# Kernel tuning notes

Hardware: AMD Instinct MI355X
Metric: run time of the kernel (lower is better)

## Reference

```python
import jax, jax.numpy as jnp
import numpy as np

B, S, D, H, E, K = 4, 1024, 1024, 16, 8, 2
DH = D // H
FF = 4 * D  # expert hidden dim
EPS = 1e-5


def _layernorm(x, g, b):
    mu = jnp.mean(x, axis=-1, keepdims=True)
    var = jnp.mean(jnp.square(x - mu), axis=-1, keepdims=True)
    return (x - mu) / jnp.sqrt(var + EPS) * g + b


def setup_inputs() -> dict:
    key = jax.random.key(0)
    ks = jax.random.split(key, 16)
    s = 0.02
    return {
        "x": jax.random.normal(ks[0], (B, S, D), jnp.float32),
        "mask": jnp.ones((B, S), jnp.int32),
        "ln1_g": jnp.ones((D,), jnp.float32),
        "ln1_b": jnp.zeros((D,), jnp.float32),
        "ln2_g": jnp.ones((D,), jnp.float32),
        "ln2_b": jnp.zeros((D,), jnp.float32),
        "wq": jax.random.normal(ks[1], (D, D), jnp.float32) * s,
        "bq": jnp.zeros((D,), jnp.float32),
        "wk": jax.random.normal(ks[2], (D, D), jnp.float32) * s,
        "bk": jnp.zeros((D,), jnp.float32),
        "wv": jax.random.normal(ks[3], (D, D), jnp.float32) * s,
        "bv": jnp.zeros((D,), jnp.float32),
        "wo": jax.random.normal(ks[4], (D, D), jnp.float32) * s,
        "bo": jnp.zeros((D,), jnp.float32),
        "w_router": jax.random.normal(ks[5], (D, E), jnp.float32) * s,
        "b_router": jnp.zeros((E,), jnp.float32),
        "w1": jax.random.normal(ks[6], (E, D, FF), jnp.float32) * s,
        "b1": jnp.zeros((E, FF), jnp.float32),
        "w2": jax.random.normal(ks[7], (E, FF, D), jnp.float32) * s,
        "b2": jnp.zeros((E, D), jnp.float32),
    }


def _forward(x, mask, ln1_g, ln1_b, ln2_g, ln2_b, wq, bq, wk, bk, wv, bv,
             wo, bo, w_router, b_router, w1, b1, w2, b2):
    scale = DH ** -0.5
    # --- attention sub-block (pre-LN) ---
    xn = _layernorm(x, ln1_g, ln1_b)
    q = (xn @ wq + bq).reshape(B, S, H, DH).transpose(0, 2, 1, 3)  # [B,H,S,DH]
    k = (xn @ wk + bk).reshape(B, S, H, DH).transpose(0, 2, 1, 3)
    v = (xn @ wv + bv).reshape(B, S, H, DH).transpose(0, 2, 1, 3)
    scores = jnp.einsum('bhqd,bhkd->bhqk', q, k) * scale
    scores = jnp.where(mask[:, None, None, :] == 0, -jnp.inf, scores)
    attn = jax.nn.softmax(scores, axis=-1)
    ao = jnp.einsum('bhqk,bhkd->bhqd', attn, v)
    ao = ao.transpose(0, 2, 1, 3).reshape(B, S, D) @ wo + bo
    x = x + ao  # dropout is identity in eval
    # --- MoE sub-block ---
    xn2 = _layernorm(x, ln2_g, ln2_b)
    logits = xn2 @ w_router + b_router          # [B,S,E]
    top_v, top_i = jax.lax.top_k(logits, K)     # [B,S,K]
    probs = jax.nn.softmax(top_v, axis=-1)      # softmax over top-k logits
    # dense combine weight per expert: sum_k prob_k * onehot(idx_k)
    combine = jnp.sum(jax.nn.one_hot(top_i, E, dtype=xn2.dtype) * probs[..., None], axis=-2)  # [B,S,E]
    h = jax.nn.gelu(jnp.einsum('bsd,edh->ebsh', xn2, w1) + b1[:, None, None, :], approximate=False)
    eo = jnp.einsum('ebsh,ehd->ebsd', h, w2) + b2[:, None, None, :]   # [E,B,S,D]
    moe_out = jnp.einsum('bse,ebsd->bsd', combine, eo)
    return x + moe_out


def reference(x, mask, ln1_g, ln1_b, ln2_g, ln2_b, wq, bq, wk, bk, wv, bv,
              wo, bo, w_router, b_router, w1, b1, w2, b2):
    return _forward(x, mask, ln1_g, ln1_b, ln2_g, ln2_b, wq, bq, wk, bk, wv,
                    bv, wo, bo, w_router, b_router, w1, b1, w2, b2)
```

## Files before the change

kernel.cpp:

```cpp
#include <hip/hip_runtime.h>
#include <hip/hip_bf16.h>
#include <cmath>

typedef __hip_bfloat16 bf16;
typedef float f32x4 __attribute__((ext_vector_type(4)));
typedef int   i32x4 __attribute__((ext_vector_type(4)));

#define DEV static __device__ __forceinline__

constexpr int BB   = 4;
constexpr int SS   = 1024;
constexpr int DM   = 1024;
constexpr int HH   = 16;
constexpr int DHD  = 64;
constexpr int NEXP = 8;
constexpr int FFD  = 4096;
constexpr int NTOK = BB*SS;
constexpr int CAP  = NTOK*2 + NEXP*128;

DEV float bf2f(unsigned short u){ union{unsigned int i; float f;} z; z.i=((unsigned int)u)<<16; return z.f; }
DEV unsigned short f2bf(float f){ bf16 h = __float2bfloat16(f); return __builtin_bit_cast(unsigned short, h); }

DEV void stage16(const void* g, void* lds_base_uniform) {
  __builtin_amdgcn_global_load_lds(
      (const __attribute__((address_space(1))) void*)g,
      (__attribute__((address_space(3))) void*)lds_base_uniform,
      16, 0, 0);
}

template<int BM,int BN,int EPI,bool EXPERT,bool GATHER,bool OUT_SLOT,int NPASS=1,int ZMODE=0>
__global__ __launch_bounds__((BM/64)*(BN/64)*64)
void et_gemm(const bf16* __restrict__ A, const bf16* __restrict__ Bt, void* __restrict__ Cout,
             const float* __restrict__ bias, const float* __restrict__ res,
             int Kdim, int lda, int ldb, int ldc,
             long abs_, long bbs_, long cbs_, float scale,
             const int* __restrict__ pad_off, const int* __restrict__ slots,
             long psA, long psB, float* __restrict__ Cf, int bias_zs)
{
  constexpr int WN = BN/64, WM = BM/64, NW = WM*WN;
  constexpr int CA = (BM/16)/NW, CB = (BN/16)/NW;
  const int tid = threadIdx.x, wid = tid>>6, lane = tid&63;

  const int gx = gridDim.x, gy = gridDim.y;
  const long nwg = (long)gx*gy*gridDim.z;
  long lin = blockIdx.x + (long)gx*(blockIdx.y + (long)gy*blockIdx.z);
  {
    const long q = nwg >> 3, r = nwg & 7;
    const long xcd = lin & 7, idx = lin >> 3;
    lin = (xcd < r ? xcd*(q+1) : r*(q+1) + (xcd-r)*q) + idx;
  }
  const int bxi = (int)(lin % gx);
  const long rem = lin / gx;
  const int byi = (int)(rem % gy);
  const int bzi = (int)(rem / gy);

  const int row0 = bxi*BM, col0 = byi*BN;
  const int z = bzi;
  int off0 = 0;
  if constexpr (EXPERT) {
    off0 = pad_off[z];
    const int rows = pad_off[z+1] - off0;
    if (row0 >= rows) return;
  }
  long coff;
  if constexpr (ZMODE==1) {
    const long hb = (long)(z>>4)*SS*DM + (long)(z&15)*64;
    A += hb; Bt += hb; coff = (long)z*SS*SS;
  } else if constexpr (ZMODE==2) {
    A  += (long)z*SS*SS;
    Bt += (long)z*DHD*SS;
    coff = (long)(z>>4)*SS*DM + (long)(z&15)*64;
  } else {
    if constexpr (!EXPERT) A += (size_t)z * abs_;
    Bt += (size_t)z * bbs_;
    coff = (long)z*cbs_;
  }
  const long bofs = (long)z * bias_zs;

  const int sr = lane>>2;
  const int sk = (lane&3)*8;

  long arow[CA];
  #pragma unroll
  for (int i=0;i<CA;i++){
    const int r = (wid + i*NW)*16 + sr;
    if constexpr (GATHER)      arow[i] = slots[off0 + row0 + r];
    else if constexpr (EXPERT) arow[i] = off0 + row0 + r;
    else                       arow[i] = row0 + r;
  }
  int brow[CB];
  #pragma unroll
  for (int i=0;i<CB;i++) brow[i] = col0 + (wid + i*NW)*16 + sr;

  const int wm = wid / WN, wn = wid % WN;
  const int fr = lane & 15, fg = lane >> 4;

  f32x4 acc[4][4];
  #pragma unroll
  for (int m=0;m<4;m++)
    #pragma unroll
    for (int n=0;n<4;n++) acc[m][n] = (f32x4)(0.f);

  if constexpr (NPASS==3) {
    __shared__ __align__(16) bf16 As[2][2][BM*32];
    __shared__ __align__(16) bf16 Bs[2][2][BN*32];
    auto STG = [&](int buf, int kt) {
      #pragma unroll
      for (int i=0;i<CA;i++){
        stage16(A +        arow[i]*(long)lda + kt + sk, (void*)&As[buf][0][(wid + i*NW)*512]);
        stage16(A + psA +  arow[i]*(long)lda + kt + sk, (void*)&As[buf][1][(wid + i*NW)*512]);
      }
      #pragma unroll
      for (int i=0;i<CB;i++){
        stage16(Bt +       (long)brow[i]*ldb + kt + sk, (void*)&Bs[buf][0][(wid + i*NW)*512]);
        stage16(Bt + psB + (long)brow[i]*ldb + kt + sk, (void*)&Bs[buf][1][(wid + i*NW)*512]);
      }
    };
    const int nsteps = Kdim >> 5;
    int cur = 0;
    STG(0, 0);
    __syncthreads();
    for (int s = 0; s < nsteps; s++) {
      if (s + 1 < nsteps) STG(cur^1, (s+1)*32);
      i32x4 a0[4], a1[4], b0[4], b1[4];
      #pragma unroll
      for (int m=0;m<4;m++) {
        a0[m] = *(const i32x4*)&As[cur][0][(wm*64 + m*16 + fr)*32 + fg*8];
        a1[m] = *(const i32x4*)&As[cur][1][(wm*64 + m*16 + fr)*32 + fg*8];
      }
      #pragma unroll
      for (int n=0;n<4;n++) {
        b0[n] = *(const i32x4*)&Bs[cur][0][(wn*64 + n*16 + fr)*32 + fg*8];
        b1[n] = *(const i32x4*)&Bs[cur][1][(wn*64 + n*16 + fr)*32 + fg*8];
      }
      asm volatile("s_nop 1" ::);
      #pragma unroll
      for (int m=0;m<4;m++)
        #pragma unroll
        for (int n=0;n<4;n++) {
          asm("v_mfma_f32_16x16x32_bf16 %0, %1, %2, %0"
              : "+v"(acc[m][n]) : "v"(a0[m]), "v"(b0[n]));
          asm("v_mfma_f32_16x16x32_bf16 %0, %1, %2, %0"
              : "+v"(acc[m][n]) : "v"(a0[m]), "v"(b1[n]));
          asm("v_mfma_f32_16x16x32_bf16 %0, %1, %2, %0"
              : "+v"(acc[m][n]) : "v"(a1[m]), "v"(b0[n]));
        }
      __syncthreads();
      cur ^= 1;
    }
  } else {
    __shared__ __align__(16) bf16 As[2][BM*32];
    __shared__ __align__(16) bf16 Bs[2][BN*32];
    auto STAGE = [&](int buf, int kt) {
      #pragma unroll
      for (int i=0;i<CA;i++)
        stage16(A + arow[i]*(long)lda + kt + sk, (void*)&As[buf][(wid + i*NW)*512]);
      #pragma unroll
      for (int i=0;i<CB;i++)
        stage16(Bt + (long)brow[i]*ldb + kt + sk, (void*)&Bs[buf][(wid + i*NW)*512]);
    };
    const int nsteps = Kdim >> 5;
    int cur = 0;
    STAGE(0, 0);
    __syncthreads();
    for (int s = 0; s < nsteps; s++) {
      if (s + 1 < nsteps) STAGE(cur^1, (s+1)*32);
      i32x4 av[4], bv[4];
      #pragma unroll
      for (int m=0;m<4;m++) av[m] = *(const i32x4*)&As[cur][(wm*64 + m*16 + fr)*32 + fg*8];
      #pragma unroll
      for (int n=0;n<4;n++) bv[n] = *(const i32x4*)&Bs[cur][(wn*64 + n*16 + fr)*32 + fg*8];
      asm volatile("s_nop 1" ::);
      #pragma unroll
      for (int m=0;m<4;m++)
        #pragma unroll
        for (int n=0;n<4;n++)
          asm("v_mfma_f32_16x16x32_bf16 %0, %1, %2, %0"
              : "+v"(acc[m][n]) : "v"(av[m]), "v"(bv[n]));
      __syncthreads();
      cur ^= 1;
    }
  }

  #pragma unroll
  for (int m=0;m<4;m++)
    #pragma unroll
    for (int n=0;n<4;n++)
      asm volatile("s_nop 7\n\ts_nop 7" : "+v"(acc[m][n]) ::);

  const long rbase = (EXPERT && OUT_SLOT) ? (long)(off0 + row0) : (long)row0;
  #pragma unroll
  for (int m=0;m<4;m++) {
    #pragma unroll
    for (int n=0;n<4;n++) {
      #pragma unroll
      for (int j=0;j<4;j++) {
        const long r = rbase + wm*64 + m*16 + fg*4 + j;
        const long c = col0 + wn*64 + n*16 + fr;
        const size_t ci = (size_t)coff + (size_t)r*ldc + c;
        float v = acc[m][n][j];
        if constexpr (EPI==0) {
          ((bf16*)Cout)[ci] = __float2bfloat16(v + bias[bofs + c]);
        } else if constexpr (EPI==1) {
          ((bf16*)Cout)[ci] = __float2bfloat16(v*scale);
        } else if constexpr (EPI==2) {
          ((float*)Cout)[ci] = v + bias[bofs + c] + res[(size_t)r*ldc + c];
        } else if constexpr (EPI==3) {
          const float t = v + bias[bofs + c];
          ((bf16*)Cout)[ci] = __float2bfloat16(0.5f*t*(1.0f+erff(t*0.70710678118654752f)));
        } else {
          const float t = v + bias[bofs + c];
          ((bf16*)Cout)[ci] = __float2bfloat16(t);
          Cf[ci] = t;
        }
      }
    }
  }
}

template<typename T>
__global__ __launch_bounds__(256)
void et_transpose(const T* __restrict__ in, bf16* __restrict__ outp,
                  int ldin, int ldout, long in_bs, long out_bs)
{
  __shared__ float tile[64][65];
  const int z = blockIdx.z;
  in   += (size_t)z * in_bs;
  outp += (size_t)z * out_bs;
  const int r0 = blockIdx.x*64, c0 = blockIdx.y*64;
  const int tid = threadIdx.x;
  #pragma unroll
  for (int i=0;i<4;i++) {
    const int idx = tid*4 + i*1024;
    const int r = idx>>6, c = idx&63;
    if constexpr (sizeof(T)==4) {
      const float4 v = *(const float4*)&in[(size_t)(r0+r)*ldin + c0 + c];
      tile[r][c]=v.x; tile[r][c+1]=v.y; tile[r][c+2]=v.z; tile[r][c+3]=v.w;
    } else {
      const ushort4 v = *(const ushort4*)&in[(size_t)(r0+r)*ldin + c0 + c];
      tile[r][c]=bf2f(v.x); tile[r][c+1]=bf2f(v.y); tile[r][c+2]=bf2f(v.z); tile[r][c+3]=bf2f(v.w);
    }
  }
  __syncthreads();
  #pragma unroll
  for (int i=0;i<4;i++) {
    const int idx = tid*4 + i*1024;
    const int c = idx>>6, r = idx&63;
    ushort4 o;
    o.x=f2bf(tile[r][c]); o.y=f2bf(tile[r+1][c]); o.z=f2bf(tile[r+2][c]); o.w=f2bf(tile[r+3][c]);
    *(ushort4*)&outp[(size_t)(c0+c)*ldout + r0 + r] = o;
  }
}

template<typename TI, typename TO>
__global__ __launch_bounds__(256)
void k_trans_head(const TI* __restrict__ in, TO* __restrict__ outp)
{
  __shared__ float tile[64][65];
  const int z = blockIdx.z;
  in   += (size_t)(z>>4)*SS*DM + (size_t)(z&15)*64;
  outp += (size_t)z*DHD*SS;
  const int r0 = blockIdx.x*64;
  const int tid = threadIdx.x;
  #pragma unroll
  for (int i=0;i<4;i++) {
    const int idx = tid*4 + i*1024;
    const int r = idx>>6, c = idx&63;
    if constexpr (sizeof(TI)==4) {
      const float4 v = *(const float4*)&in[(size_t)(r0+r)*DM + c];
      tile[r][c]=v.x; tile[r][c+1]=v.y; tile[r][c+2]=v.z; tile[r][c+3]=v.w;
    } else {
      const ushort4 v = *(const ushort4*)&in[(size_t)(r0+r)*DM + c];
      tile[r][c]=bf2f(v.x); tile[r][c+1]=bf2f(v.y); tile[r][c+2]=bf2f(v.z); tile[r][c+3]=bf2f(v.w);
    }
  }
  __syncthreads();
  #pragma unroll
  for (int i=0;i<4;i++) {
    const int idx = tid*4 + i*1024;
    const int c = idx>>6, r = idx&63;
    if constexpr (sizeof(TO)==4) {
      float4 o;
      o.x=tile[r][c]; o.y=tile[r+1][c]; o.z=tile[r+2][c]; o.w=tile[r+3][c];
      *(float4*)&outp[(size_t)c*SS + r0 + r] = o;
    } else {
      ushort4 o;
      o.x=f2bf(tile[r][c]); o.y=f2bf(tile[r+1][c]); o.z=f2bf(tile[r+2][c]); o.w=f2bf(tile[r+3][c]);
      *(ushort4*)&outp[(size_t)c*SS + r0 + r] = o;
    }
  }
}

__global__ __launch_bounds__(256)
void et_transpose2(const float* __restrict__ in0, const float* __restrict__ in1,
                   const float* __restrict__ in2, bf16* __restrict__ outp,
                   int ldin, int ldout, long pstride, long out_zs)
{
  __shared__ float tile[64][65];
  const int z = blockIdx.z;
  const float* in = (z==0) ? in0 : (z==1) ? in1 : in2;
  outp += (size_t)z * out_zs;
  const int r0 = blockIdx.x*64, c0 = blockIdx.y*64;
  const int tid = threadIdx.x;
  #pragma unroll
  for (int i=0;i<4;i++) {
    const int idx = tid*4 + i*1024;
    const int r = idx>>6, c = idx&63;
    const float4 v = *(const float4*)&in[(size_t)(r0+r)*ldin + c0 + c];
    tile[r][c]=v.x; tile[r][c+1]=v.y; tile[r][c+2]=v.z; tile[r][c+3]=v.w;
  }
  __syncthreads();
  #pragma unroll
  for (int i=0;i<4;i++) {
    const int idx = tid*4 + i*1024;
    const int c = idx>>6, r = idx&63;
    ushort4 o0, o1;
    unsigned short* p0 = (unsigned short*)&o0;
    unsigned short* p1 = (unsigned short*)&o1;
    #pragma unroll
    for (int j=0;j<4;j++) {
      float v = tile[r+j][c];
      const unsigned short h0 = f2bf(v);
      p0[j] = h0;
      v -= bf2f(h0);
      p1[j] = f2bf(v);
    }
    const size_t oi = (size_t)(c0+c)*ldout + r0 + r;
    *(ushort4*)&outp[oi] = o0;
    *(ushort4*)&outp[oi + pstride] = o1;
  }
}

__global__ __launch_bounds__(256)
void et_ln2(const float* __restrict__ xin, const float* __restrict__ g,
            const float* __restrict__ bsh, bf16* __restrict__ outp, long pstride)
{
  const int row = blockIdx.x, tid = threadIdx.x;
  const float4 v = ((const float4*)(xin + (size_t)row*DM))[tid];
  float s = v.x+v.y+v.z+v.w;
  #pragma unroll
  for (int o=32;o;o>>=1) s += __shfl_xor(s,o);
  __shared__ float s4[4], q4[4];
  if ((tid&63)==0) s4[tid>>6]=s;
  __syncthreads();
  const float mu = (s4[0]+s4[1]+s4[2]+s4[3]) * (1.f/DM);
  const float d0=v.x-mu,d1=v.y-mu,d2=v.z-mu,d3=v.w-mu;
  float q = d0*d0+d1*d1+d2*d2+d3*d3;
  #pragma unroll
  for (int o=32;o;o>>=1) q += __shfl_xor(q,o);
  if ((tid&63)==0) q4[tid>>6]=q;
  __syncthreads();
  const float var = (q4[0]+q4[1]+q4[2]+q4[3]) * (1.f/DM);
  const float rstd = rsqrtf(var + 1e-5f);
  const float4 gg = ((const float4*)g)[tid];
  const float4 bb = ((const float4*)bsh)[tid];
  float of[4];
  of[0] = d0*rstd*gg.x + bb.x;
  of[1] = d1*rstd*gg.y + bb.y;
  of[2] = d2*rstd*gg.z + bb.z;
  of[3] = d3*rstd*gg.w + bb.w;
  ushort4 p0, p1;
  unsigned short* pp0 = (unsigned short*)&p0;
  unsigned short* pp1 = (unsigned short*)&p1;
  #pragma unroll
  for (int k=0;k<4;k++) {
    float vv = of[k];
    const unsigned short h0 = f2bf(vv); pp0[k] = h0;
    vv -= bf2f(h0);
    pp1[k] = f2bf(vv);
  }
  const size_t oi = (size_t)row*DM;
  ((ushort4*)(outp + oi))[tid] = p0;
  ((ushort4*)(outp + pstride + oi))[tid] = p1;
}

__global__ __launch_bounds__(256)
void et_softmax(bf16* __restrict__ scp, const int* __restrict__ mask)
{
  const int row = blockIdx.x, tid = threadIdx.x;
  const int b = row >> 14;
  bf16* rp = scp + (size_t)row*SS;
  const int* mrow = mask + (size_t)b*SS;
  const ushort4 u = ((const ushort4*)rp)[tid];
  const int4 mv = ((const int4*)mrow)[tid];
  float f0 = bf2f(u.x), f1 = bf2f(u.y), f2 = bf2f(u.z), f3 = bf2f(u.w);
  if (mv.x==0) f0 = -1e30f;
  if (mv.y==0) f1 = -1e30f;
  if (mv.z==0) f2 = -1e30f;
  if (mv.w==0) f3 = -1e30f;
  float m = fmaxf(fmaxf(f0,f1),fmaxf(f2,f3));
  #pragma unroll
  for (int o=32;o;o>>=1) m = fmaxf(m, __shfl_xor(m,o));
  __shared__ float sm[4], ssum[4];
  if ((tid&63)==0) sm[tid>>6] = m;
  __syncthreads();
  m = fmaxf(fmaxf(sm[0],sm[1]),fmaxf(sm[2],sm[3]));
  const float e0 = __expf(f0-m), e1 = __expf(f1-m), e2 = __expf(f2-m), e3 = __expf(f3-m);
  float s = e0+e1+e2+e3;
  #pragma unroll
  for (int o=32;o;o>>=1) s += __shfl_xor(s,o);
  if ((tid&63)==0) ssum[tid>>6] = s;
  __syncthreads();
  s = ssum[0]+ssum[1]+ssum[2]+ssum[3];
  const float ri = 1.0f/s;
  ushort4 o4;
  o4.x = f2bf(e0*ri); o4.y = f2bf(e1*ri); o4.z = f2bf(e2*ri); o4.w = f2bf(e3*ri);
  ((ushort4*)rp)[tid] = o4;
}

__global__ __launch_bounds__(256)
void et_router2(const float* __restrict__ x1, const float* __restrict__ g,
                const float* __restrict__ bsh, const float* __restrict__ wr,
                const float* __restrict__ br, bf16* __restrict__ xn2,
                int* __restrict__ t2e, float* __restrict__ t2p,
                int* __restrict__ flaglist, int* __restrict__ cntb)
{
  const int wid = threadIdx.x>>6, lane = threadIdx.x&63;
  const int t = blockIdx.x*4 + wid;
  const float* xr = x1 + (size_t)t*DM;
  float4 xv[4];
  float s = 0.f;
  #pragma unroll
  for (int p=0;p<4;p++){
    xv[p] = *(const float4*)&xr[p*256 + lane*4];
    s += xv[p].x+xv[p].y+xv[p].z+xv[p].w;
  }
  #pragma unroll
  for (int o=32;o;o>>=1) s += __shfl_xor(s,o);
  const float mu = s * (1.f/DM);
  float q = 0.f;
  #pragma unroll
  for (int p=0;p<4;p++){
    const float a=xv[p].x-mu,b=xv[p].y-mu,c=xv[p].z-mu,d=xv[p].w-mu;
    q += a*a+b*b+c*c+d*d;
  }
  #pragma unroll
  for (int o=32;o;o>>=1) q += __shfl_xor(q,o);
  const float rstd = rsqrtf(q*(1.f/DM) + 1e-5f);
  float acc[NEXP];
  #pragma unroll
  for (int e=0;e<NEXP;e++) acc[e]=0.f;
  #pragma unroll
  for (int p=0;p<4;p++){
    const int d0 = p*256 + lane*4;
    const float4 gg = *(const float4*)&g[d0];
    const float4 bb = *(const float4*)&bsh[d0];
    float xn[4];
    xn[0]=(xv[p].x-mu)*rstd*gg.x+bb.x;
    xn[1]=(xv[p].y-mu)*rstd*gg.y+bb.y;
    xn[2]=(xv[p].z-mu)*rstd*gg.z+bb.z;
    xn[3]=(xv[p].w-mu)*rstd*gg.w+bb.w;
    ushort4 xo;
    xo.x=f2bf(xn[0]); xo.y=f2bf(xn[1]); xo.z=f2bf(xn[2]); xo.w=f2bf(xn[3]);
    *(ushort4*)&xn2[(size_t)t*DM + d0] = xo;
    #pragma unroll
    for (int j=0;j<4;j++){
      const float4 w0  = ((const float4*)&wr[(size_t)(d0+j)*NEXP])[0];
      const float4 w1v = ((const float4*)&wr[(size_t)(d0+j)*NEXP])[1];
      acc[0]+=xn[j]*w0.x;  acc[1]+=xn[j]*w0.y;  acc[2]+=xn[j]*w0.z;  acc[3]+=xn[j]*w0.w;
      acc[4]+=xn[j]*w1v.x; acc[5]+=xn[j]*w1v.y; acc[6]+=xn[j]*w1v.z; acc[7]+=xn[j]*w1v.w;
    }
  }
  #pragma unroll
  for (int e=0;e<NEXP;e++)
    #pragma unroll
    for (int o=32;o;o>>=1) acc[e] += __shfl_xor(acc[e],o);
  if (lane==0) {
    float v0=-1e30f, v1=-1e30f, v2=-1e30f; int e0=0, e1=0;
    #pragma unroll
    for (int e=0;e<NEXP;e++) {
      const float v = acc[e] + br[e];
      if (v>v0){v2=v1;v1=v0;e1=e0;v0=v;e0=e;}
      else if (v>v1){v2=v1;v1=v;e1=e;}
      else if (v>v2){v2=v;}
    }
    const float dd = __expf(v1-v0);
    const float p0 = 1.f/(1.f+dd);
    t2e[t*2]=e0; t2e[t*2+1]=e1;
    t2p[t*2]=p0; t2p[t*2+1]=dd*p0;
    if (v1 - v2 < 0.02f) {
      const int b = t >> 10;
      const int ib = atomicAdd(&cntb[b], 1);
      flaglist[b*1024 + ib] = t;
    }
  }
}

__global__ __launch_bounds__(256)
void k_rec4(const float* __restrict__ qf, const float* __restrict__ kfT,
            const float* __restrict__ vf, const int* __restrict__ flaglist,
            const int* __restrict__ cntb, const int* __restrict__ mask,
            float* __restrict__ aoF)
{
  const int h = blockIdx.y, b = blockIdx.z;
  const int tid = threadIdx.x, lane = tid&63, wv_ = tid>>6;
  const int nb = cntb[b];
  __shared__ float qs[4][64];
  __shared__ float scb[4][SS];
  __shared__ float part[4][4][64];
  __shared__ float tsum[4];
  const int* mrow = mask + (size_t)b*SS;
  const float* kbase = kfT + ((size_t)(b*HH + h)*DHD)*SS + tid;
  const float* vbase = vf + (size_t)b*SS*DM + h*64 + lane;

  for (int t0 = blockIdx.x*4; t0 < nb; t0 += gridDim.x*4) {
    const int nt = min(4, nb - t0);
    for (int idx = tid; idx < 4*64; idx += 256) {
      const int j = idx >> 6, d = idx & 63;
      float qv = 0.f;
      if (j < nt) {
        const int t = flaglist[b*1024 + t0 + j];
        qv = qf[(size_t)t*DM + h*64 + d];
      }
      qs[j][d] = qv;
    }
    __syncthreads();
    float a00=0,a01=0,a02=0,a03=0, a10=0,a11=0,a12=0,a13=0;
    float a20=0,a21=0,a22=0,a23=0, a30=0,a31=0,a32=0,a33=0;
    #pragma unroll 4
    for (int u=0; u<64; u++) {
      const float* kr = kbase + (size_t)u*SS;
      const float k0 = kr[0], k1 = kr[256], k2 = kr[512], k3 = kr[768];
      const float q0 = qs[0][u], q1 = qs[1][u], q2 = qs[2][u], q3 = qs[3][u];
      a00 += q0*k0; a01 += q0*k1; a02 += q0*k2; a03 += q0*k3;
      a10 += q1*k0; a11 += q1*k1; a12 += q1*k2; a13 += q1*k3;
      a20 += q2*k0; a21 += q2*k1; a22 += q2*k2; a23 += q2*k3;
      a30 += q3*k0; a31 += q3*k1; a32 += q3*k2; a33 += q3*k3;
    }
    const bool m0 = mrow[tid]!=0, m1 = mrow[tid+256]!=0, m2 = mrow[tid+512]!=0, m3 = mrow[tid+768]!=0;
    scb[0][tid]=m0?a00*0.125f:-1e30f; scb[0][tid+256]=m1?a01*0.125f:-1e30f;
    scb[0][tid+512]=m2?a02*0.125f:-1e30f; scb[0][tid+768]=m3?a03*0.125f:-1e30f;
    scb[1][tid]=m0?a10*0.125f:-1e30f; scb[1][tid+256]=m1?a11*0.125f:-1e30f;
    scb[1][tid+512]=m2?a12*0.125f:-1e30f; scb[1][tid+768]=m3?a13*0.125f:-1e30f;
    scb[2][tid]=m0?a20*0.125f:-1e30f; scb[2][tid+256]=m1?a21*0.125f:-1e30f;
    scb[2][tid+512]=m2?a22*0.125f:-1e30f; scb[2][tid+768]=m3?a23*0.125f:-1e30f;
    scb[3][tid]=m0?a30*0.125f:-1e30f; scb[3][tid+256]=m1?a31*0.125f:-1e30f;
    scb[3][tid+512]=m2?a32*0.125f:-1e30f; scb[3][tid+768]=m3?a33*0.125f:-1e30f;
    __syncthreads();
    {
      const int j = wv_;
      float v[16];
      float lm = -1e30f;
      #pragma unroll
      for (int kk=0;kk<16;kk++) { v[kk] = scb[j][lane + kk*64]; lm = fmaxf(lm, v[kk]); }
      #pragma unroll
      for (int o=32;o;o>>=1) lm = fmaxf(lm, __shfl_xor(lm,o));
      float ls = 0.f;
      #pragma unroll
      for (int kk=0;kk<16;kk++) {
        const float e = expf(v[kk]-lm);
        scb[j][lane + kk*64] = e; ls += e;
      }
      #pragma unroll
      for (int o=32;o;o>>=1) ls += __shfl_xor(ls,o);
      if (lane==0) tsum[j] = ls;
    }
    __syncthreads();
    float p0=0.f, p1=0.f, p2=0.f, p3=0.f;
    for (int s = wv_*4; s < SS; s += 16) {
      const float v0 = vbase[(size_t) s   *DM];
      const float v1 = vbase[(size_t)(s+1)*DM];
      const float v2 = vbase[(size_t)(s+2)*DM];
      const float v3 = vbase[(size_t)(s+3)*DM];
      p0 += scb[0][s]*v0 + scb[0][s+1]*v1 + scb[0][s+2]*v2 + scb[0][s+3]*v3;
      p1 += scb[1][s]*v0 + scb[1][s+1]*v1 + scb[1][s+2]*v2 + scb[1][s+3]*v3;
      p2 += scb[2][s]*v0 + scb[2][s+1]*v1 + scb[2][s+2]*v2 + scb[2][s+3]*v3;
      p3 += scb[3][s]*v0 + scb[3][s+1]*v1 + scb[3][s+2]*v2 + scb[3][s+3]*v3;
    }
    part[wv_][0][lane] = p0;
    part[wv_][1][lane] = p1;
    part[wv_][2][lane] = p2;
    part[wv_][3][lane] = p3;
    __syncthreads();
    for (int idx = tid; idx < nt*64; idx += 256) {
      const int j = idx >> 6, d = idx & 63;
      aoF[(size_t)(b*1024 + t0 + j)*DM + h*64 + d] =
        (part[0][j][d]+part[1][j][d]+part[2][j][d]+part[3][j][d]) / tsum[j];
    }
    __syncthreads();
  }
}

__global__ __launch_bounds__(256)
void k_flag_proj2(const float* __restrict__ aoF, const float* __restrict__ wo,
                  const float* __restrict__ bo, const float* __restrict__ x,
                  const int* __restrict__ flaglist, const int* __restrict__ cntb,
                  float* __restrict__ yF)
{
  const int tile = blockIdx.x;
  const int b = tile >> 7;
  const int i0 = (tile & 127) * 8;
  const int nb = cntb[b];
  if (i0 >= nb) return;
  const int nt = min(8, nb - i0);
  const int c0 = blockIdx.y * 128;
  const int tid = threadIdx.x;
  const int c = c0 + (tid & 127);
  const int dh = tid >> 7;
  __shared__ float ar[8][DM];
  __shared__ float ph[2][8][128];
  for (int k = tid; k < 8*256; k += 256) {
    const int j = k >> 8, q4i = k & 255;
    float4 v = make_float4(0.f,0.f,0.f,0.f);
    if (j < nt) v = ((const float4*)(aoF + (size_t)(b*1024 + i0 + j)*DM))[q4i];
    ((float4*)ar[j])[q4i] = v;
  }
  __syncthreads();
  float acc0=0.f, acc1=0.f, acc2=0.f, acc3=0.f;
  float acc4=0.f, acc5=0.f, acc6=0.f, acc7=0.f;
  const int dbase = dh*512;
  #pragma unroll 4
  for (int d=0; d<512; d++) {
    const float w = wo[(size_t)(dbase+d)*DM + c];
    acc0 += ar[0][dbase+d]*w; acc1 += ar[1][dbase+d]*w;
    acc2 += ar[2][dbase+d]*w; acc3 += ar[3][dbase+d]*w;
    acc4 += ar[4][dbase+d]*w; acc5 += ar[5][dbase+d]*w;
    acc6 += ar[6][dbase+d]*w; acc7 += ar[7][dbase+d]*w;
  }
  const int lc = tid & 127;
  ph[dh][0][lc]=acc0; ph[dh][1][lc]=acc1; ph[dh][2][lc]=acc2; ph[dh][3][lc]=acc3;
  ph[dh][4][lc]=acc4; ph[dh][5][lc]=acc5; ph[dh][6][lc]=acc6; ph[dh][7][lc]=acc7;
  __syncthreads();
  for (int k = tid; k < nt*128; k += 256) {
    const int j = k >> 7, ccl = k & 127;
    const int cc = c0 + ccl;
    const int slot = b*1024 + i0 + j;
    const int t = flaglist[slot];
    yF[(size_t)slot*DM + cc] = ph[0][j][ccl] + ph[1][j][ccl] + bo[cc] + x[(size_t)t*DM + cc];
  }
}

__global__ __launch_bounds__(256)
void k_flag_router(const float* __restrict__ yF, const float* __restrict__ g,
                   const float* __restrict__ bsh, const float* __restrict__ wr,
                   const float* __restrict__ br, const int* __restrict__ flaglist,
                   const int* __restrict__ cntb, int* __restrict__ t2e,
                   float* __restrict__ t2p)
{
  const int tid = threadIdx.x, lane = tid&63, wv_ = tid>>6;
  __shared__ float s4[4], q4[4], pt[4][8];
  for (int idx = blockIdx.x; idx < NTOK; idx += gridDim.x) {
    const int b = idx >> 10, ib = idx & 1023;
    if (ib >= cntb[b]) continue;
    const int t = flaglist[idx];
    const float4 v = ((const float4*)(yF + (size_t)idx*DM))[tid];
    float s = v.x+v.y+v.z+v.w;
    #pragma unroll
    for (int o=32;o;o>>=1) s += __shfl_xor(s,o);
    if (lane==0) s4[wv_]=s;
    __syncthreads();
    const float mu = (s4[0]+s4[1]+s4[2]+s4[3])*(1.f/DM);
    const float d0=v.x-mu, d1=v.y-mu, d2=v.z-mu, d3=v.w-mu;
    float q = d0*d0+d1*d1+d2*d2+d3*d3;
    #pragma unroll
    for (int o=32;o;o>>=1) q += __shfl_xor(q,o);
    if (lane==0) q4[wv_]=q;
    __syncthreads();
    const float var = (q4[0]+q4[1]+q4[2]+q4[3])*(1.f/DM);
    const float rstd = 1.0f/sqrtf(var + 1e-5f);
    const int dbase = tid*4;
    const float4 gg = ((const float4*)g)[tid];
    const float4 bb = ((const float4*)bsh)[tid];
    const float x0 = d0*rstd*gg.x+bb.x, x1_ = d1*rstd*gg.y+bb.y;
    const float x2 = d2*rstd*gg.z+bb.z, x3_ = d3*rstd*gg.w+bb.w;
    float pl[8];
    #pragma unroll
    for (int e=0;e<8;e++)
      pl[e] = x0*wr[(size_t)(dbase+0)*8+e] + x1_*wr[(size_t)(dbase+1)*8+e]
            + x2*wr[(size_t)(dbase+2)*8+e] + x3_*wr[(size_t)(dbase+3)*8+e];
    #pragma unroll
    for (int e=0;e<8;e++)
      #pragma unroll
      for (int o=32;o;o>>=1) pl[e] += __shfl_xor(pl[e],o);
    if (lane==0) {
      #pragma unroll
      for (int e=0;e<8;e++) pt[wv_][e]=pl[e];
    }
    __syncthreads();
    if (tid==0) {
      float v0=-1e30f, v1=-1e30f; int e0=0, e1=0;
      for (int e=0;e<8;e++) {
        const float L = pt[0][e]+pt[1][e]+pt[2][e]+pt[3][e] + br[e];
        if (L>v0){v1=v0;e1=e0;v0=L;e0=e;}
        else if (L>v1){v1=L;e1=e;}
      }
      const float dd=expf(v1-v0), p0=1.f/(1.f+dd);
      t2e[t*2]=e0; t2e[t*2+1]=e1;
      t2p[t*2]=p0; t2p[t*2+1]=dd*p0;
    }
    __syncthreads();
  }
}

__global__ void et_init(const float* __restrict__ bq, const float* __restrict__ bk,
                        const float* __restrict__ bv, float* __restrict__ bcat,
                        int* __restrict__ cnt)
{
  const int i = blockIdx.x*256 + threadIdx.x;
  if (i < 16) cnt[i]=0;
  if (i < DM) { bcat[i]=bq[i]; bcat[DM+i]=bk[i]; bcat[2*DM+i]=bv[i]; }
}

__global__ void et_count(const int* __restrict__ t2e, int* __restrict__ cnt)
{
  const int t = blockIdx.x*256 + threadIdx.x;
  if (t < NTOK) {
    atomicAdd(&cnt[t2e[t*2]], 1);
    atomicAdd(&cnt[t2e[t*2+1]], 1);
  }
}

__global__ void et_scan(const int* __restrict__ cnt, int* __restrict__ poff,
                        int* __restrict__ fil, int* __restrict__ slots)
{
  const int tid = threadIdx.x;
  if (tid==0) {
    int o=0;
    for (int e=0;e<NEXP;e++){ poff[e]=o; o += ((cnt[e]+127)>>7)<<7; }
    poff[NEXP]=o;
  }
  if (tid<NEXP) fil[tid]=0;
  for (int i=tid;i<CAP;i+=256) slots[i]=0;
}

__global__ void et_fill(const int* __restrict__ t2e, const int* __restrict__ poff,
                        int* __restrict__ fil, int* __restrict__ slots, int* __restrict__ sof)
{
  const int t = blockIdx.x*256 + threadIdx.x;
  if (t >= NTOK) return;
  #pragma unroll
  for (int kk=0;kk<2;kk++) {
    const int e = t2e[t*2+kk];
    const int pos = atomicAdd(&fil[e], 1);
    const int sl = poff[e] + pos;
    slots[sl] = t;
    sof[t*2+kk] = sl;
  }
}

__global__ __launch_bounds__(256)
void et_combine(const float* __restrict__ x1, const bf16* __restrict__ eo,
                const float* __restrict__ t2p, const int* __restrict__ sof,
                float* __restrict__ outp)
{
  const int t = blockIdx.x, tid = threadIdx.x;
  const int s0 = sof[t*2], s1 = sof[t*2+1];
  const float p0 = t2p[t*2], p1 = t2p[t*2+1];
  const float4 xv = ((const float4*)(x1 + (size_t)t*DM))[tid];
  const ushort4 a = ((const ushort4*)(eo + (size_t)s0*DM))[tid];
  const ushort4 c = ((const ushort4*)(eo + (size_t)s1*DM))[tid];
  float4 o;
  o.x = xv.x + p0*bf2f(a.x) + p1*bf2f(c.x);
  o.y = xv.y + p0*bf2f(a.y) + p1*bf2f(c.y);
  o.z = xv.z + p0*bf2f(a.z) + p1*bf2f(c.z);
  o.w = xv.w + p0*bf2f(a.w) + p1*bf2f(c.w);
  ((float4*)(outp + (size_t)t*DM))[tid] = o;
}

extern "C" void kernel_launch(void* const* d_in, const int* in_sizes, int n_in,
                              void* d_out, int out_size, void* d_ws, size_t ws_size,
                              hipStream_t stream)
{
  (void)in_sizes; (void)n_in; (void)out_size; (void)ws_size;
  const float* x    = (const float*)d_in[0];
  const int*   mask = (const int*)  d_in[1];
  const float* ln1g = (const float*)d_in[2];
  const float* ln1b = (const float*)d_in[3];
  const float* ln2g = (const float*)d_in[4];
  const float* ln2b = (const float*)d_in[5];
  const float* wq   = (const float*)d_in[6];
  const float* bq   = (const float*)d_in[7];
  const float* wk   = (const float*)d_in[8];
  const float* bk   = (const float*)d_in[9];
  const float* wv   = (const float*)d_in[10];
  const float* bv   = (const float*)d_in[11];
  const float* wo   = (const float*)d_in[12];
  const float* bo   = (const float*)d_in[13];
  const float* wr   = (const float*)d_in[14];
  const float* br   = (const float*)d_in[15];
  const float* w1   = (const float*)d_in[16];
  const float* b1   = (const float*)d_in[17];
  const float* w2   = (const float*)d_in[18];
  const float* b2   = (const float*)d_in[19];
  float* outp = (float*)d_out;

  char* wsb = (char*)d_ws;
  size_t off = 0;
  auto alloc = [&](size_t bytes)->void* {
    void* p = wsb + off;
    off += (bytes + 255) & ~(size_t)255;
    return p;
  };
  const long WPS  = (long)DM*DM;
  const long XPS  = (long)NTOK*DM;
  const long EWS  = (long)DM*FFD;
  bf16*  wqT2  = (bf16*) alloc((size_t)2*WPS*2);
  bf16*  wkT2  = (bf16*) alloc((size_t)2*WPS*2);
  bf16*  wvT2  = (bf16*) alloc((size_t)2*WPS*2);
  bf16*  woT   = (bf16*) alloc((size_t)WPS*2);
  bf16*  w1Ta  = (bf16*) alloc((size_t)NEXP*EWS*2);
  bf16*  w2Ta  = (bf16*) alloc((size_t)NEXP*EWS*2);
  bf16*  xn2p  = (bf16*) alloc((size_t)2*XPS*2);
  bf16*  qb    = (bf16*) alloc((size_t)XPS*2);
  bf16*  kb    = (bf16*) alloc((size_t)XPS*2);
  bf16*  vb    = (bf16*) alloc((size_t)XPS*2);
  bf16*  vt    = (bf16*) alloc((size_t)XPS*2);
  float* qf    = (float*)alloc((size_t)XPS*4);
  float* kf    = (float*)alloc((size_t)XPS*4);
  float* vf    = (float*)alloc((size_t)XPS*4);
  float* kfT   = (float*)alloc((size_t)XPS*4);
  bf16*  aob   = (bf16*) alloc((size_t)XPS*2);
  float* x1    = (float*)alloc((size_t)XPS*4);
  bf16*  xn2   = (bf16*) alloc((size_t)XPS*2);
  bf16*  hbuf  = (bf16*) alloc((size_t)CAP*FFD*2);
  bf16*  eo    = (bf16*) alloc((size_t)CAP*DM*2);
  float* bcat  = (float*)alloc((size_t)3*DM*4);
  int*   t2e   = (int*)  alloc((size_t)NTOK*2*4);
  float* t2p   = (float*)alloc((size_t)NTOK*2*4);
  int*   slots = (int*)  alloc((size_t)CAP*4);
  int*   sof   = (int*)  alloc((size_t)NTOK*2*4);
  int*   flagl = (int*)  alloc((size_t)NTOK*4);
  int*   cnt   = (int*)  alloc(64);
  int*   fil   = (int*)  alloc(64);
  int*   poff  = (int*)  alloc(64);
  int*   cntb  = cnt + 8;
  bf16*  sc    = (bf16*) w1Ta;
  float* aoF   = (float*)qb;
  float* yF    = (float*)vb;

  const dim3 T256(256);

  et_init<<<4,T256,0,stream>>>(bq, bk, bv, bcat, cnt);
  et_transpose2<<<dim3(DM/64,DM/64,3),T256,0,stream>>>(wq, wk, wv, wqT2, DM, DM, WPS, 2*WPS);
  et_transpose<float><<<dim3(DM/64,DM/64,1),T256,0,stream>>>(wo, woT, DM, DM, 0, 0);

  et_ln2<<<NTOK,T256,0,stream>>>(x, ln1g, ln1b, xn2p, XPS);

  et_gemm<128,64,4,false,false,false,3,0><<<dim3(NTOK/128, DM/64, 3),dim3(128),0,stream>>>(
      xn2p, wqT2, qb, bcat, nullptr, DM, DM, DM, DM,
      0, 2*WPS, XPS, 1.f, nullptr, nullptr, XPS, WPS, qf, DM);

  k_trans_head<bf16,bf16><<<dim3(SS/64,1,BB*HH),T256,0,stream>>>(vb, vt);
  k_trans_head<float,float><<<dim3(SS/64,1,BB*HH),T256,0,stream>>>(kf, kfT);

  et_gemm<128,128,1,false,false,false,1,1><<<dim3(SS/128, SS/128, BB*HH),T256,0,stream>>>(
      qb, kb, sc, nullptr, nullptr, DHD, DM, DM, SS,
      0,0,0, 0.125f, nullptr,nullptr, 0,0,nullptr, 0);
  et_softmax<<<BB*HH*SS,T256,0,stream>>>(sc, mask);
  et_gemm<64,64,1,false,false,false,1,2><<<dim3(SS/64, 1, BB*HH),dim3(64),0,stream>>>(
      sc, vt, aob, nullptr, nullptr, SS, SS, SS, DM,
      0,0,0, 1.0f, nullptr,nullptr, 0,0,nullptr, 0);

  et_gemm<64,64,2,false,false,false,1,0><<<dim3(NTOK/64, DM/64, 1),dim3(64),0,stream>>>(
      aob, woT, x1, bo, x, DM, DM, DM, DM, 0,0,0, 1.f, nullptr,nullptr, 0,0,nullptr, 0);

  et_router2<<<NTOK/4,T256,0,stream>>>(x1, ln2g, ln2b, wr, br, xn2, t2e, t2p, flagl, cntb);
  k_rec4<<<dim3(32,HH,BB),T256,0,stream>>>(qf, kfT, vf, flagl, cntb, mask, aoF);
  k_flag_proj2<<<dim3(NTOK/8, DM/128),T256,0,stream>>>(aoF, wo, bo, x, flagl, cntb, yF);
  k_flag_router<<<1024,T256,0,stream>>>(yF, ln2g, ln2b, wr, br, flagl, cntb, t2e, t2p);

  et_count<<<NTOK/256,T256,0,stream>>>(t2e, cnt);
  et_scan<<<1,T256,0,stream>>>(cnt, poff, fil, slots);
  et_fill<<<NTOK/256,T256,0,stream>>>(t2e, poff, fil, slots, sof);

  et_transpose<float><<<dim3(DM/64, FFD/64, NEXP),T256,0,stream>>>(w1, w1Ta, FFD, DM, EWS, EWS);
  et_transpose<float><<<dim3(FFD/64, DM/64, NEXP),T256,0,stream>>>(w2, w2Ta, DM, FFD, EWS, EWS);

  et_gemm<128,128,3,true,true,true,1,0><<<dim3(NTOK/128, FFD/128, NEXP),T256,0,stream>>>(
      xn2, w1Ta, hbuf, b1, nullptr, DM, DM, DM, FFD,
      0, EWS, 0, 1.f, poff, slots, 0,0,nullptr, FFD);
  et_gemm<128,128,0,true,false,true,1,0><<<dim3(NTOK/128, DM/128, NEXP),T256,0,stream>>>(
      hbuf, w2Ta, eo, b2, nullptr, FFD, FFD, FFD, DM,
      0, EWS, 0, 1.f, poff, nullptr, 0,0,nullptr, DM);

  et_combine<<<NTOK,T256,0,stream>>>(x1, eo, t2p, sof, outp);
}
```

Baseline: 922.3 us.

## Fuse QK^T, softmax and PV into a single flash-attention kernel

Replaces the three-kernel attention path (score GEMM writing a full bf16 score matrix, row softmax kernel, PV GEMM) with one online-softmax kernel. Each block keeps a 64-row query tile in registers and streams K and V tiles through swizzled LDS. It computes scores with MFMA, tracks running max and sum per row, and accumulates the output. This removes the B*H*S*S score round trip to global memory and two kernel launches. In exchange, P is rounded to bf16 per tile, K/V loads are synchronous with no double buffering, and only 4 waves per block hide latency.

```diff
diff --git a/kernel.cpp b/kernel.cpp
--- a/kernel.cpp
+++ b/kernel.cpp
@@ -63,10 +63,7 @@
     if (row0 >= rows) return;
   }
   long coff;
-  if constexpr (ZMODE==1) {
-    const long hb = (long)(z>>4)*SS*DM + (long)(z&15)*64;
-    A += hb; Bt += hb; coff = (long)z*SS*SS;
-  } else if constexpr (ZMODE==2) {
+  if constexpr (ZMODE==2) {
     A  += (long)z*SS*SS;
     Bt += (long)z*DHD*SS;
     coff = (long)(z>>4)*SS*DM + (long)(z&15)*64;
@@ -218,6 +215,130 @@
   }
 }
 
+__global__ __launch_bounds__(256)
+void k_flash(const bf16* __restrict__ qb, const bf16* __restrict__ kb,
+             const bf16* __restrict__ vt, const int* __restrict__ mask,
+             bf16* __restrict__ aob)
+{
+  const int qt = blockIdx.x, h = blockIdx.y, b = blockIdx.z;
+  const int tid = threadIdx.x, wid = tid>>6, lane = tid&63;
+  const int fr = lane & 15, fg = lane >> 4;
+  __shared__ __align__(16) bf16 Ks[64*64];
+  __shared__ __align__(16) bf16 Vs[64*64];
+  __shared__ __align__(16) bf16 Pl[4][16*64];
+  const int q0 = qt*64;
+  const int qrow = q0 + wid*16 + fr;
+  i32x4 qreg[2];
+  #pragma unroll
+  for (int c=0;c<2;c++)
+    qreg[c] = *(const i32x4*)&qb[((size_t)(b*SS)+qrow)*DM + h*64 + c*32 + fg*8];
+  f32x4 oacc[4];
+  #pragma unroll
+  for (int n=0;n<4;n++) oacc[n]=(f32x4)(0.f);
+  float mrow[4], lrow[4];
+  #pragma unroll
+  for (int j=0;j<4;j++){ mrow[j]=-1e30f; lrow[j]=0.f; }
+
+  const int srow = lane>>3;
+  const int scolsw = ((lane&7) ^ srow)*8;
+  auto swz = [](int row, int coleb)->int {
+    return row*128 + (coleb ^ ((row&7)<<4));
+  };
+
+  for (int kt=0; kt<SS/64; kt++) {
+    const int kv0 = kt*64;
+    #pragma unroll
+    for (int i=0;i<2;i++) {
+      const int r = (wid*2+i)*8 + srow;
+      stage16(kb + ((size_t)(b*SS)+kv0+r)*DM + h*64 + scolsw, (void*)&Ks[(wid*2+i)*512]);
+      stage16(vt + ((size_t)(b*HH+h)*64 + r)*SS + kv0 + scolsw, (void*)&Vs[(wid*2+i)*512]);
+    }
+    __syncthreads();
+    f32x4 sacc[4];
+    #pragma unroll
+    for (int n=0;n<4;n++) sacc[n]=(f32x4)(0.f);
+    asm volatile("s_nop 1" ::);
+    #pragma unroll
+    for (int c=0;c<2;c++) {
+      i32x4 bk[4];
+      #pragma unroll
+      for (int n=0;n<4;n++)
+        bk[n] = *(const i32x4*)((const char*)Ks + swz(n*16+fr, c*64+fg*16));
+      #pragma unroll
+      for (int n=0;n<4;n++)
+        asm("v_mfma_f32_16x16x32_bf16 %0, %1, %2, %0"
+            : "+v"(sacc[n]) : "v"(qreg[c]), "v"(bk[n]));
+    }
+    #pragma unroll
+    for (int n=0;n<4;n++)
+      asm volatile("s_nop 7\n\ts_nop 7" : "+v"(sacc[n]) ::);
+    float sc[4][4];
+    #pragma unroll
+    for (int n=0;n<4;n++) {
+      const bool mm = mask[b*SS + kv0 + n*16 + fr] != 0;
+      #pragma unroll
+      for (int j=0;j<4;j++)
+        sc[n][j] = mm ? sacc[n][j]*0.125f : -1e30f;
+    }
+    float scale[4];
+    #pragma unroll
+    for (int j=0;j<4;j++) {
+      float tm = fmaxf(fmaxf(sc[0][j],sc[1][j]),fmaxf(sc[2][j],sc[3][j]));
+      #pragma unroll
+      for (int o=8;o;o>>=1) tm = fmaxf(tm, __shfl_xor(tm,o));
+      const float nm = fmaxf(mrow[j], tm);
+      scale[j] = __expf(mrow[j]-nm);
+      mrow[j] = nm;
+      float ts = 0.f;
+      #pragma unroll
+      for (int n=0;n<4;n++) { sc[n][j] = __expf(sc[n][j]-nm); ts += sc[n][j]; }
+      #pragma unroll
+      for (int o=8;o;o>>=1) ts += __shfl_xor(ts,o);
+      lrow[j] = lrow[j]*scale[j] + ts;
+    }
+    #pragma unroll
+    for (int n=0;n<4;n++)
+      asm volatile("s_nop 7\n\ts_nop 7" : "+v"(oacc[n]) ::);
+    #pragma unroll
+    for (int n=0;n<4;n++)
+      #pragma unroll
+      for (int j=0;j<4;j++) oacc[n][j] *= scale[j];
+    char* plw = (char*)Pl[wid];
+    #pragma unroll
+    for (int n=0;n<4;n++)
+      #pragma unroll
+      for (int j=0;j<4;j++) {
+        const int row = fg*4+j, col = n*16+fr;
+        *(bf16*)(plw + row*128 + ((col*2) ^ ((row&7)<<4))) = __float2bfloat16(sc[n][j]);
+      }
+    asm volatile("s_nop 1" ::);
+    #pragma unroll
+    for (int c=0;c<2;c++) {
+      i32x4 pa = *(const i32x4*)(plw + swz(fr, c*64+fg*16));
+      i32x4 bv[4];
+      #pragma unroll
+      for (int n=0;n<4;n++)
+        bv[n] = *(const i32x4*)((const char*)Vs + swz(n*16+fr, c*64+fg*16));
+      #pragma unroll
+      for (int n=0;n<4;n++)
+        asm("v_mfma_f32_16x16x32_bf16 %0, %1, %2, %0"
+            : "+v"(oacc[n]) : "v"(pa), "v"(bv[n]));
+    }
+    __syncthreads();
+  }
+  #pragma unroll
+  for (int n=0;n<4;n++)
+    asm volatile("s_nop 7\n\ts_nop 7" : "+v"(oacc[n]) ::);
+  #pragma unroll
+  for (int j=0;j<4;j++) {
+    const float ri = 1.0f / lrow[j];
+    const size_t rbase = ((size_t)(b*SS) + q0 + wid*16 + fg*4 + j)*DM + h*64;
+    #pragma unroll
+    for (int n=0;n<4;n++)
+      aob[rbase + n*16 + fr] = __float2bfloat16(oacc[n][j] * ri);
+  }
+}
+
 template<typename T>
 __global__ __launch_bounds__(256)
 void et_transpose(const T* __restrict__ in, bf16* __restrict__ outp,
@@ -372,40 +493,6 @@
   const size_t oi = (size_t)row*DM;
   ((ushort4*)(outp + oi))[tid] = p0;
   ((ushort4*)(outp + pstride + oi))[tid] = p1;
-}
-
-__global__ __launch_bounds__(256)
-void et_softmax(bf16* __restrict__ scp, const int* __restrict__ mask)
-{
-  const int row = blockIdx.x, tid = threadIdx.x;
-  const int b = row >> 14;
-  bf16* rp = scp + (size_t)row*SS;
-  const int* mrow = mask + (size_t)b*SS;
-  const ushort4 u = ((const ushort4*)rp)[tid];
-  const int4 mv = ((const int4*)mrow)[tid];
-  float f0 = bf2f(u.x), f1 = bf2f(u.y), f2 = bf2f(u.z), f3 = bf2f(u.w);
-  if (mv.x==0) f0 = -1e30f;
-  if (mv.y==0) f1 = -1e30f;
-  if (mv.z==0) f2 = -1e30f;
-  if (mv.w==0) f3 = -1e30f;
-  float m = fmaxf(fmaxf(f0,f1),fmaxf(f2,f3));
-  #pragma unroll
-  for (int o=32;o;o>>=1) m = fmaxf(m, __shfl_xor(m,o));
-  __shared__ float sm[4], ssum[4];
-  if ((tid&63)==0) sm[tid>>6] = m;
-  __syncthreads();
-  m = fmaxf(fmaxf(sm[0],sm[1]),fmaxf(sm[2],sm[3]));
-  const float e0 = __expf(f0-m), e1 = __expf(f1-m), e2 = __expf(f2-m), e3 = __expf(f3-m);
-  float s = e0+e1+e2+e3;
-  #pragma unroll
-  for (int o=32;o;o>>=1) s += __shfl_xor(s,o);
-  if ((tid&63)==0) ssum[tid>>6] = s;
-  __syncthreads();
-  s = ssum[0]+ssum[1]+ssum[2]+ssum[3];
-  const float ri = 1.0f/s;
-  ushort4 o4;
-  o4.x = f2bf(e0*ri); o4.y = f2bf(e1*ri); o4.z = f2bf(e2*ri); o4.w = f2bf(e3*ri);
-  ((ushort4*)rp)[tid] = o4;
 }
 
 __global__ __launch_bounds__(256)
@@ -824,7 +911,6 @@
   int*   fil   = (int*)  alloc(64);
   int*   poff  = (int*)  alloc(64);
   int*   cntb  = cnt + 8;
-  bf16*  sc    = (bf16*) w1Ta;
   float* aoF   = (float*)qb;
   float* yF    = (float*)vb;
 
@@ -843,13 +929,7 @@
   k_trans_head<bf16,bf16><<<dim3(SS/64,1,BB*HH),T256,0,stream>>>(vb, vt);
   k_trans_head<float,float><<<dim3(SS/64,1,BB*HH),T256,0,stream>>>(kf, kfT);
 
-  et_gemm<128,128,1,false,false,false,1,1><<<dim3(SS/128, SS/128, BB*HH),T256,0,stream>>>(
-      qb, kb, sc, nullptr, nullptr, DHD, DM, DM, SS,
-      0,0,0, 0.125f, nullptr,nullptr, 0,0,nullptr, 0);
-  et_softmax<<<BB*HH*SS,T256,0,stream>>>(sc, mask);
-  et_gemm<64,64,1,false,false,false,1,2><<<dim3(SS/64, 1, BB*HH),dim3(64),0,stream>>>(
-      sc, vt, aob, nullptr, nullptr, SS, SS, SS, DM,
-      0,0,0, 1.0f, nullptr,nullptr, 0,0,nullptr, 0);
+  k_flash<<<dim3(SS/64, HH, BB),T256,0,stream>>>(qb, kb, vt, mask, aob);
 
   et_gemm<64,64,2,false,false,false,1,0><<<dim3(NTOK/64, DM/64, 1),dim3(64),0,stream>>>(
       aob, woT, x1, bo, x, DM, DM, DM, DM, 0,0,0, 1.f, nullptr,nullptr, 0,0,nullptr, 0);
```

Measured after the change: 826.8 us, median of 4. 10.4% less time.
